# Performance work log

Hardware: AMD Instinct MI355X
Metric: run time of the kernel (lower is better)

## Reference

```python
import jax, jax.numpy as jnp
import numpy as np
from jax import lax

VOCAB = 27
N_EMBD = 512
D_MODEL = 256
PAD_IDX = 26
OUT = 1
B, T = 256, 512


def _lstm_layer(x, w_ih, w_hh, b_ih, b_hh):
    # x: [B, T, in]; w_ih: [4H, in]; w_hh: [4H, H]
    Bb = x.shape[0]
    H = w_hh.shape[1]
    # precompute input contribution to all gates for all timesteps
    xg = jnp.einsum('bti,gi->btg', x, w_ih) + b_ih + b_hh  # [B, T, 4H]

    def step(carry, xg_t):
        h, c = carry
        g = xg_t + h @ w_hh.T  # [B, 4H]
        i, f, gg, o = jnp.split(g, 4, axis=-1)  # PyTorch gate order i,f,g,o
        i = jax.nn.sigmoid(i)
        f = jax.nn.sigmoid(f)
        gg = jnp.tanh(gg)
        o = jax.nn.sigmoid(o)
        c = f * c + i * gg
        h = o * jnp.tanh(c)
        return (h, c), h

    h0 = jnp.zeros((Bb, H), dtype=x.dtype)
    c0 = jnp.zeros((Bb, H), dtype=x.dtype)
    _, ys = lax.scan(step, (h0, c0), jnp.swapaxes(xg, 0, 1))
    return jnp.swapaxes(ys, 0, 1)  # [B, T, H]


def setup_inputs() -> dict:
    key = jax.random.key(0)
    ks = jax.random.split(key, 16)
    s_e = 1.0  # nn.Embedding default init is N(0,1)
    emb = jax.random.normal(ks[0], (VOCAB, N_EMBD), dtype=jnp.float32)
    emb = emb.at[PAD_IDX].set(0.0)
    bound = 1.0 / np.sqrt(D_MODEL)

    def u(k, shape, b):
        return jax.random.uniform(k, shape, dtype=jnp.float32, minval=-b, maxval=b)

    inp = {
        'input_ids': jax.random.randint(ks[1], (B, T), 0, VOCAB, dtype=jnp.int64)
                      if jax.config.jax_enable_x64 else
                      jax.random.randint(ks[1], (B, T), 0, VOCAB).astype(jnp.int32),
        'emb': emb,
        'w_ih0': u(ks[2], (4 * D_MODEL, N_EMBD), bound),
        'w_hh0': u(ks[3], (4 * D_MODEL, D_MODEL), bound),
        'b_ih0': u(ks[4], (4 * D_MODEL,), bound),
        'b_hh0': u(ks[5], (4 * D_MODEL,), bound),
        'w_ih1': u(ks[6], (4 * D_MODEL, D_MODEL), bound),
        'w_hh1': u(ks[7], (4 * D_MODEL, D_MODEL), bound),
        'b_ih1': u(ks[8], (4 * D_MODEL,), bound),
        'b_hh1': u(ks[9], (4 * D_MODEL,), bound),
        'fc1_w': u(ks[10], (D_MODEL // 2, D_MODEL), bound),
        'fc1_b': u(ks[11], (D_MODEL // 2,), bound),
        'fc2_w': u(ks[12], (OUT, D_MODEL // 2), 1.0 / np.sqrt(D_MODEL // 2)),
        'fc2_b': u(ks[13], (OUT,), 1.0 / np.sqrt(D_MODEL // 2)),
    }
    return inp


def reference(input_ids, emb, w_ih0, w_hh0, b_ih0, b_hh0,
              w_ih1, w_hh1, b_ih1, b_hh1, fc1_w, fc1_b, fc2_w, fc2_b):
    # embedding with padding_idx: pad row forced to zero
    table = emb.at[PAD_IDX].set(0.0)
    x = table[input_ids]  # [B, T, n_embd]
    h1 = _lstm_layer(x, w_ih0, w_hh0, b_ih0, b_hh0)   # [B, T, H]
    h2 = _lstm_layer(h1, w_ih1, w_hh1, b_ih1, b_hh1)  # [B, T, H]
    last = h2[:, -1, :]                                # [B, H]
    hidden = jax.nn.relu(last @ fc1_w.T + fc1_b)
    logits = hidden @ fc2_w.T + fc2_b                  # [B, 1]
    return logits
```

## Files before the change

### kernel.cpp

```cpp
#include <hip/hip_runtime.h>

typedef unsigned short u16;
typedef unsigned int u32;
typedef unsigned long long u64;

#define BATCH 256
#define TT 512
#define HID 256
#define GATES 1024
#define NEMB 512
#define VOC 27
#define HPAD 260

__device__ __forceinline__ float bf1(u16 x){ union{u32 u; float f;} v; v.u = ((u32)x) << 16; return v.f; }
__device__ __forceinline__ u16 f2bf(float f){
  union{float f; u32 u;} v; v.f = f;
  u32 u = v.u;
  return (u16)((u + 0x7fffu + ((u >> 16) & 1u)) >> 16);
}
__device__ __forceinline__ float sigm(float x){ return 1.f / (1.f + __expf(-x)); }

__global__ void k_detect(const u16* __restrict__ b, int* __restrict__ flag) {
  int bad = 0;
  for (int k = threadIdx.x; k < 512; k += 64)
    if (((b[2 * k] >> 7) & 0xFF) >= 127) bad = 1;
  unsigned long long m = __ballot(bad);
  if (threadIdx.x == 0) flag[0] = (m != 0ULL) ? 0 : 1;
}

__global__ void k_convert(const void* __restrict__ src, float* __restrict__ dst,
                          int n, const int* __restrict__ flag) {
  int i = blockIdx.x * 256 + threadIdx.x;
  if (i >= n) return;
  dst[i] = flag[0] ? bf1(((const u16*)src)[i]) : ((const float*)src)[i];
}

__global__ void k_prep(const void* __restrict__ emb, const void* __restrict__ wih,
                       const void* __restrict__ bih, const void* __restrict__ bhh,
                       const int* __restrict__ flag, float* __restrict__ W0) {
  int idx = blockIdx.x * 256 + threadIdx.x;
  if (idx >= VOC * GATES) return;
  int v = idx >> 10, g = idx & (GATES - 1);
  int isbf = flag[0];
  float acc = isbf ? (bf1(((const u16*)bih)[g]) + bf1(((const u16*)bhh)[g]))
                   : (((const float*)bih)[g] + ((const float*)bhh)[g]);
  if (v != 26) {
    float s = 0.f;
    if (isbf) {
      const u16* e = (const u16*)emb + v * NEMB;
      const u16* w = (const u16*)wih + g * NEMB;
      for (int i = 0; i < NEMB; i++) s = fmaf(bf1(e[i]), bf1(w[i]), s);
    } else {
      const float* e = (const float*)emb + v * NEMB;
      const float* w = (const float*)wih + g * NEMB;
      for (int i = 0; i < NEMB; i++) s = fmaf(e[i], w[i], s);
    }
    acc += s;
  }
  W0[idx] = acc;
}

__global__ __launch_bounds__(1024) void k_lstm(
    const int* __restrict__ ids, const float* __restrict__ W0,
    const float* __restrict__ whh0, const float* __restrict__ wih1,
    const float* __restrict__ whh1,
    const float* __restrict__ bih1, const float* __restrict__ bhh1,
    float* __restrict__ h0a, float* __restrict__ h0b,
    float* __restrict__ h1a, float* __restrict__ h1b,
    u32* __restrict__ bar)
{
  const int tid = threadIdx.x;
  const int bid = blockIdx.x;
  const int xcd = bid & 7, m = bid >> 3;
  const int bg = xcd * 2 + (m & 1);
  const int jc = m >> 1;

  const int tb = tid & 15;
  const int rr = tid >> 4;
  const int grow = ((rr >> 4) << 8) + (jc << 4) + (rr & 15);

  __shared__ float hp0[16][HPAD];
  __shared__ float hp1[16][HPAD];
  __shared__ float gs0[64][16];
  __shared__ float gs1[64][16];
  __shared__ int   ids_s[16];

  const float* wl0 = whh0 + (size_t)grow * HID;
  const float* wi  = wih1 + (size_t)grow * HID;
  const float* wh  = whh1 + (size_t)grow * HID;
  const float bsum = bih1[grow] + bhh1[grow];

  const int lay = tid >> 8;
  const int pb = tid & 15, pj = (tid >> 4) & 15;
  const int prow = (bg * 16 + pb) * HID + (jc * 16 + pj);
  float cr = 0.f;

  u32* cnt = bar + bg * 32;

  for (int t = 0; t <= TT; ++t) {
    const float* h0p = ((t + 1) & 1) ? h0b : h0a;
    float*       h0n = (t & 1) ? h0b : h0a;
    const float* h1p = (t & 1) ? h1b : h1a;
    float*       h1n = ((t + 1) & 1) ? h1b : h1a;

    {
      const u64* s0base = (const u64*)(h0p + bg * 16 * HID);
      const u64* s1base = (const u64*)(h1p + bg * 16 * HID);
      #pragma unroll
      for (int u = 0; u < 2; ++u) {
        int e = tid + 1024 * u;
        int sb = e >> 7, sk = e & 127;
        u64 v0 = __hip_atomic_load(s0base + e, __ATOMIC_RELAXED, __HIP_MEMORY_SCOPE_AGENT);
        u64 v1 = __hip_atomic_load(s1base + e, __ATOMIC_RELAXED, __HIP_MEMORY_SCOPE_AGENT);
        *(u64*)&hp0[sb][sk * 2] = v0;
        *(u64*)&hp1[sb][sk * 2] = v1;
      }
      if (t < TT && tid < 16) ids_s[tid] = ids[(bg * 16 + tid) * TT + t];
    }
    __syncthreads();

    if (t < TT) {
      float a = W0[(size_t)ids_s[tb] * GATES + grow];
      const float* hh = hp0[tb];
      #pragma unroll 8
      for (int k = 0; k < HID; k += 4) {
        float4 q = *(const float4*)(wl0 + k);
        float4 hv = *(const float4*)(hh + k);
        a = fmaf(q.x, hv.x, a); a = fmaf(q.y, hv.y, a);
        a = fmaf(q.z, hv.z, a); a = fmaf(q.w, hv.w, a);
      }
      gs0[rr][tb] = a;
    }

    if (t > 0) {
      float e0 = bsum, e1 = 0.f;
      const float* xx = hp0[tb];
      const float* hh = hp1[tb];
      #pragma unroll 8
      for (int k = 0; k < HID; k += 4) {
        float4 qi = *(const float4*)(wi + k);
        float4 qh = *(const float4*)(wh + k);
        float4 xv = *(const float4*)(xx + k);
        float4 hv = *(const float4*)(hh + k);
        e0 = fmaf(qi.x, xv.x, e0); e0 = fmaf(qi.y, xv.y, e0);
        e0 = fmaf(qi.z, xv.z, e0); e0 = fmaf(qi.w, xv.w, e0);
        e1 = fmaf(qh.x, hv.x, e1); e1 = fmaf(qh.y, hv.y, e1);
        e1 = fmaf(qh.z, hv.z, e1); e1 = fmaf(qh.w, hv.w, e1);
      }
      gs1[rr][tb] = e0 + e1;
    }
    __syncthreads();

    if (tid < 512) {
      bool act = lay ? (t > 0) : (t < TT);
      if (act) {
        float (*gs)[16] = lay ? gs1 : gs0;
        float gi = sigm(gs[pj][pb]);
        float gf = sigm(gs[16 + pj][pb]);
        float gg = tanhf(gs[32 + pj][pb]);
        float go = sigm(gs[48 + pj][pb]);
        cr = fmaf(gf, cr, gi * gg);
        float* hn = lay ? h1n : h0n;
        __hip_atomic_store(&hn[prow], go * tanhf(cr),
                           __ATOMIC_RELAXED, __HIP_MEMORY_SCOPE_AGENT);
      }
    }

    if (t < TT) {
      __syncthreads();
      if (tid == 0) {
        __hip_atomic_fetch_add(cnt, 1u, __ATOMIC_RELAXED, __HIP_MEMORY_SCOPE_AGENT);
        u32 want = (u32)(16 * (t + 1));
        while (__hip_atomic_load(cnt, __ATOMIC_RELAXED, __HIP_MEMORY_SCOPE_AGENT) < want)
          __builtin_amdgcn_s_sleep(1);
      }
      __syncthreads();
    }
  }
}

__global__ __launch_bounds__(128) void k_fc(
    const float* __restrict__ hfin,
    const void* __restrict__ fc1w, const void* __restrict__ fc1b,
    const void* __restrict__ fc2w, const void* __restrict__ fc2b,
    const int* __restrict__ flag, void* __restrict__ out) {
  int b = blockIdx.x, j = threadIdx.x;
  __shared__ float red[128];
  const float* h = hfin + b * HID;
  int isbf = flag[0];
  float acc = isbf ? bf1(((const u16*)fc1b)[j]) : ((const float*)fc1b)[j];
  if (isbf) {
    const u16* w = (const u16*)fc1w + j * HID;
    for (int k = 0; k < HID; k++) acc = fmaf(bf1(w[k]), h[k], acc);
  } else {
    const float* w = (const float*)fc1w + j * HID;
    for (int k = 0; k < HID; k++) acc = fmaf(w[k], h[k], acc);
  }
  acc = fmaxf(acc, 0.f);
  float w2 = isbf ? bf1(((const u16*)fc2w)[j]) : ((const float*)fc2w)[j];
  red[j] = acc * w2;
  __syncthreads();
  for (int s = 64; s > 0; s >>= 1) {
    if (j < s) red[j] += red[j + s];
    __syncthreads();
  }
  if (j == 0) {
    float b2 = isbf ? bf1(((const u16*)fc2b)[0]) : ((const float*)fc2b)[0];
    float r = red[0] + b2;
    if (isbf) ((u16*)out)[b] = f2bf(r);
    else      ((float*)out)[b] = r;
  }
}

extern "C" void kernel_launch(void* const* d_in, const int* in_sizes, int n_in,
                              void* d_out, int out_size, void* d_ws, size_t ws_size,
                              hipStream_t stream) {
  const int* ids   = (const int*)d_in[0];
  const void* emb  = d_in[1];
  const void* wih0 = d_in[2];
  const void* whh0 = d_in[3];
  const void* bih0 = d_in[4];
  const void* bhh0 = d_in[5];
  const void* wih1 = d_in[6];
  const void* whh1 = d_in[7];
  const void* bih1 = d_in[8];
  const void* bhh1 = d_in[9];
  const void* fc1w = d_in[10];
  const void* fc1b = d_in[11];
  const void* fc2w = d_in[12];
  const void* fc2b = d_in[13];

  float* ws = (float*)d_ws;
  int*   flag    = (int*)ws;
  float* W0emb   = ws + 16;
  float* whh0_f  = W0emb  + VOC * GATES;
  float* wih1_f  = whh0_f + GATES * HID;
  float* whh1_f  = wih1_f + GATES * HID;
  float* bih1_f  = whh1_f + GATES * HID;
  float* bhh1_f  = bih1_f + GATES;
  float* h0A = bhh1_f + GATES;
  float* h0B = h0A + BATCH * HID;
  float* c0  = h0B + BATCH * HID;
  float* h1A = c0  + BATCH * HID;
  float* h1B = h1A + BATCH * HID;
  float* c1  = h1B + BATCH * HID;
  u32*   bar = (u32*)c0;

  k_detect<<<1, 64, 0, stream>>>((const u16*)bih0, flag);

  k_convert<<<(GATES * HID + 255) / 256, 256, 0, stream>>>(whh0, whh0_f, GATES * HID, flag);
  k_convert<<<(GATES * HID + 255) / 256, 256, 0, stream>>>(wih1, wih1_f, GATES * HID, flag);
  k_convert<<<(GATES * HID + 255) / 256, 256, 0, stream>>>(whh1, whh1_f, GATES * HID, flag);
  k_convert<<<(GATES + 255) / 256, 256, 0, stream>>>(bih1, bih1_f, GATES, flag);
  k_convert<<<(GATES + 255) / 256, 256, 0, stream>>>(bhh1, bhh1_f, GATES, flag);

  hipMemsetAsync(h0A, 0, (size_t)6 * BATCH * HID * sizeof(float), stream);

  k_prep<<<(VOC * GATES + 255) / 256, 256, 0, stream>>>(emb, wih0, bih0, bhh0, flag, W0emb);

  k_lstm<<<256, 1024, 0, stream>>>(ids, W0emb, whh0_f, wih1_f, whh1_f,
                                   bih1_f, bhh1_f, h0A, h0B, h1A, h1B, bar);

  k_fc<<<BATCH, 128, 0, stream>>>(h1B, fc1w, fc1b, fc2w, fc2b, flag, d_out);
}
```

Baseline: 13.39 ms.

## Split LSTM layer barriers and skew layer-1 to overlap with layer-0 signaling

Gives the two stacked LSTM layers separate group counters. Layer 0 signals as soon as its new hidden state is stored, so other blocks can proceed while layer 1 computes; layer 1 now runs two steps behind and reads double-buffered layer-0 states. It also preloads all token ids into shared memory, pads the gate scratch arrays to avoid bank conflicts, and uses packed 2-wide FMAs for the dot products. The price is more barriers per step, a larger shared-memory footprint (the ids table alone is about 32KB), and tricky buffer-parity correctness across the skewed layers.

```diff
diff --git a/kernel.cpp b/kernel.cpp
--- a/kernel.cpp
+++ b/kernel.cpp
@@ -3,6 +3,7 @@
 typedef unsigned short u16;
 typedef unsigned int u32;
 typedef unsigned long long u64;
+typedef float f32x2 __attribute__((ext_vector_type(2)));
 
 #define BATCH 256
 #define TT 512
@@ -19,6 +20,8 @@
   return (u16)((u + 0x7fffu + ((u >> 16) & 1u)) >> 16);
 }
 __device__ __forceinline__ float sigm(float x){ return 1.f / (1.f + __expf(-x)); }
+__device__ __forceinline__ f32x2 lo2(float4 v){ f32x2 r; r.x = v.x; r.y = v.y; return r; }
+__device__ __forceinline__ f32x2 hi2(float4 v){ f32x2 r; r.x = v.z; r.y = v.w; return r; }
 
 __global__ void k_detect(const u16* __restrict__ b, int* __restrict__ flag) {
   int bad = 0;
@@ -79,103 +82,130 @@
   const int rr = tid >> 4;
   const int grow = ((rr >> 4) << 8) + (jc << 4) + (rr & 15);
 
-  __shared__ float hp0[16][HPAD];
-  __shared__ float hp1[16][HPAD];
-  __shared__ float gs0[64][16];
-  __shared__ float gs1[64][16];
-  __shared__ int   ids_s[16];
+  __shared__ __align__(16) float hp0[2][16][HPAD];
+  __shared__ __align__(16) float hp1[16][HPAD];
+  __shared__ float gs0[64][17];
+  __shared__ float gs1[64][17];
+  __shared__ int   ids_l[16][TT + 1];
 
   const float* wl0 = whh0 + (size_t)grow * HID;
   const float* wi  = wih1 + (size_t)grow * HID;
   const float* wh  = whh1 + (size_t)grow * HID;
   const float bsum = bih1[grow] + bhh1[grow];
 
-  const int lay = tid >> 8;
-  const int pb = tid & 15, pj = (tid >> 4) & 15;
+  const int pj = tid & 15, pb = (tid >> 4) & 15;
   const int prow = (bg * 16 + pb) * HID + (jc * 16 + pj);
-  float cr = 0.f;
-
-  u32* cnt = bar + bg * 32;
-
-  for (int t = 0; t <= TT; ++t) {
-    const float* h0p = ((t + 1) & 1) ? h0b : h0a;
-    float*       h0n = (t & 1) ? h0b : h0a;
-    const float* h1p = (t & 1) ? h1b : h1a;
-    float*       h1n = ((t + 1) & 1) ? h1b : h1a;
-
-    {
-      const u64* s0base = (const u64*)(h0p + bg * 16 * HID);
-      const u64* s1base = (const u64*)(h1p + bg * 16 * HID);
+  float c0r = 0.f, c1r = 0.f;
+
+  u32* cnt0 = bar + bg * 64;
+  u32* cnt1 = cnt0 + 32;
+
+  #pragma unroll
+  for (int u = 0; u < 8; ++u) {
+    int e = tid + 1024 * u;
+    int b = e >> 9, tt = e & 511;
+    ids_l[b][tt] = ids[(bg * 16 + b) * TT + tt];
+  }
+
+  for (int t = 0; t <= TT + 1; ++t) {
+    if (tid == 0) {
+      if (t >= 1 && t <= TT) {
+        u32 want = 16u * (u32)t;
+        while (__hip_atomic_load(cnt0, __ATOMIC_RELAXED, __HIP_MEMORY_SCOPE_AGENT) < want)
+          __builtin_amdgcn_s_sleep(1);
+      }
+      if (t >= 3) {
+        u32 want = 16u * (u32)(t - 2);
+        while (__hip_atomic_load(cnt1, __ATOMIC_RELAXED, __HIP_MEMORY_SCOPE_AGENT) < want)
+          __builtin_amdgcn_s_sleep(1);
+      }
+    }
+    __syncthreads();
+
+    if (t <= TT) {
+      const float* h0p = ((t + 1) & 1) ? h0b : h0a;
+      const u64* s0 = (const u64*)(h0p + bg * 16 * HID);
+      float (*dst)[HPAD] = hp0[t & 1];
       #pragma unroll
       for (int u = 0; u < 2; ++u) {
         int e = tid + 1024 * u;
-        int sb = e >> 7, sk = e & 127;
-        u64 v0 = __hip_atomic_load(s0base + e, __ATOMIC_RELAXED, __HIP_MEMORY_SCOPE_AGENT);
-        u64 v1 = __hip_atomic_load(s1base + e, __ATOMIC_RELAXED, __HIP_MEMORY_SCOPE_AGENT);
-        *(u64*)&hp0[sb][sk * 2] = v0;
-        *(u64*)&hp1[sb][sk * 2] = v1;
-      }
-      if (t < TT && tid < 16) ids_s[tid] = ids[(bg * 16 + tid) * TT + t];
+        u64 v = __hip_atomic_load(s0 + e, __ATOMIC_RELAXED, __HIP_MEMORY_SCOPE_AGENT);
+        *(u64*)&dst[e >> 7][(e & 127) * 2] = v;
+      }
+    }
+    if (t >= 2) {
+      const float* h1p = ((t + 1) & 1) ? h1b : h1a;
+      const u64* s1 = (const u64*)(h1p + bg * 16 * HID);
+      #pragma unroll
+      for (int u = 0; u < 2; ++u) {
+        int e = tid + 1024 * u;
+        u64 v = __hip_atomic_load(s1 + e, __ATOMIC_RELAXED, __HIP_MEMORY_SCOPE_AGENT);
+        *(u64*)&hp1[e >> 7][(e & 127) * 2] = v;
+      }
     }
     __syncthreads();
 
     if (t < TT) {
-      float a = W0[(size_t)ids_s[tb] * GATES + grow];
-      const float* hh = hp0[tb];
+      float xgv = W0[(size_t)ids_l[tb][t] * GATES + grow];
+      const float4* w4 = (const float4*)wl0;
+      const float4* h4 = (const float4*)hp0[t & 1][tb];
+      f32x2 sA = {0.f, 0.f}, sB = {0.f, 0.f};
       #pragma unroll 8
-      for (int k = 0; k < HID; k += 4) {
-        float4 q = *(const float4*)(wl0 + k);
-        float4 hv = *(const float4*)(hh + k);
-        a = fmaf(q.x, hv.x, a); a = fmaf(q.y, hv.y, a);
-        a = fmaf(q.z, hv.z, a); a = fmaf(q.w, hv.w, a);
-      }
-      gs0[rr][tb] = a;
-    }
-
-    if (t > 0) {
-      float e0 = bsum, e1 = 0.f;
-      const float* xx = hp0[tb];
-      const float* hh = hp1[tb];
+      for (int k = 0; k < 64; ++k) {
+        float4 q = w4[k], hv = h4[k];
+        sA = lo2(q) * lo2(hv) + sA;
+        sB = hi2(q) * hi2(hv) + sB;
+      }
+      gs0[rr][tb] = xgv + sA.x + sA.y + sB.x + sB.y;
+    }
+    __syncthreads();
+
+    if (t < TT && tid < 256) {
+      float gi = sigm(gs0[pj][pb]);
+      float gf = sigm(gs0[16 + pj][pb]);
+      float gg = tanhf(gs0[32 + pj][pb]);
+      float go = sigm(gs0[48 + pj][pb]);
+      c0r = fmaf(gf, c0r, gi * gg);
+      float* h0n = (t & 1) ? h0b : h0a;
+      __hip_atomic_store(&h0n[prow], go * tanhf(c0r),
+                         __ATOMIC_RELAXED, __HIP_MEMORY_SCOPE_AGENT);
+    }
+    __syncthreads();
+    if (tid == 0 && t < TT)
+      __hip_atomic_fetch_add(cnt0, 1u, __ATOMIC_RELAXED, __HIP_MEMORY_SCOPE_AGENT);
+
+    if (t >= 2) {
+      const float4* wi4 = (const float4*)wi;
+      const float4* wh4 = (const float4*)wh;
+      const float4* x4  = (const float4*)hp0[(t - 1) & 1][tb];
+      const float4* h4  = (const float4*)hp1[tb];
+      f32x2 sIa = {0.f,0.f}, sIb = {0.f,0.f}, sHa = {0.f,0.f}, sHb = {0.f,0.f};
       #pragma unroll 8
-      for (int k = 0; k < HID; k += 4) {
-        float4 qi = *(const float4*)(wi + k);
-        float4 qh = *(const float4*)(wh + k);
-        float4 xv = *(const float4*)(xx + k);
-        float4 hv = *(const float4*)(hh + k);
-        e0 = fmaf(qi.x, xv.x, e0); e0 = fmaf(qi.y, xv.y, e0);
-        e0 = fmaf(qi.z, xv.z, e0); e0 = fmaf(qi.w, xv.w, e0);
-        e1 = fmaf(qh.x, hv.x, e1); e1 = fmaf(qh.y, hv.y, e1);
-        e1 = fmaf(qh.z, hv.z, e1); e1 = fmaf(qh.w, hv.w, e1);
-      }
-      gs1[rr][tb] = e0 + e1;
-    }
-    __syncthreads();
-
-    if (tid < 512) {
-      bool act = lay ? (t > 0) : (t < TT);
-      if (act) {
-        float (*gs)[16] = lay ? gs1 : gs0;
-        float gi = sigm(gs[pj][pb]);
-        float gf = sigm(gs[16 + pj][pb]);
-        float gg = tanhf(gs[32 + pj][pb]);
-        float go = sigm(gs[48 + pj][pb]);
-        cr = fmaf(gf, cr, gi * gg);
-        float* hn = lay ? h1n : h0n;
-        __hip_atomic_store(&hn[prow], go * tanhf(cr),
-                           __ATOMIC_RELAXED, __HIP_MEMORY_SCOPE_AGENT);
-      }
-    }
-
-    if (t < TT) {
-      __syncthreads();
-      if (tid == 0) {
-        __hip_atomic_fetch_add(cnt, 1u, __ATOMIC_RELAXED, __HIP_MEMORY_SCOPE_AGENT);
-        u32 want = (u32)(16 * (t + 1));
-        while (__hip_atomic_load(cnt, __ATOMIC_RELAXED, __HIP_MEMORY_SCOPE_AGENT) < want)
-          __builtin_amdgcn_s_sleep(1);
-      }
-      __syncthreads();
-    }
+      for (int k = 0; k < 64; ++k) {
+        float4 qi = wi4[k], qh = wh4[k], xv = x4[k], hv = h4[k];
+        sIa = lo2(qi) * lo2(xv) + sIa;
+        sIb = hi2(qi) * hi2(xv) + sIb;
+        sHa = lo2(qh) * lo2(hv) + sHa;
+        sHb = hi2(qh) * hi2(hv) + sHb;
+      }
+      gs1[rr][tb] = bsum + sIa.x + sIa.y + sIb.x + sIb.y
+                         + sHa.x + sHa.y + sHb.x + sHb.y;
+    }
+    __syncthreads();
+
+    if (t >= 2 && tid < 256) {
+      float gi = sigm(gs1[pj][pb]);
+      float gf = sigm(gs1[16 + pj][pb]);
+      float gg = tanhf(gs1[32 + pj][pb]);
+      float go = sigm(gs1[48 + pj][pb]);
+      c1r = fmaf(gf, c1r, gi * gg);
+      float* h1n = (t & 1) ? h1b : h1a;
+      __hip_atomic_store(&h1n[prow], go * tanhf(c1r),
+                         __ATOMIC_RELAXED, __HIP_MEMORY_SCOPE_AGENT);
+    }
+    __syncthreads();
+    if (tid == 0 && t >= 2 && t <= TT)
+      __hip_atomic_fetch_add(cnt1, 1u, __ATOMIC_RELAXED, __HIP_MEMORY_SCOPE_AGENT);
   }
 }
 
```

Measured after the change: 13.15 ms. Within noise of the previous version (-1.8%).

## Replace cross-block barrier LSTM with per-block batch ownership and local state

Applied to the files above, without the earlier changes.

The recurrent kernel now gives each of 64 blocks four full batch rows, so the hidden state stays in shared memory and the global atomic barrier between blocks is gone. Each thread computes all four gates for one hidden unit over a quarter of K, using packed float2 FMAs, and the partial sums are reduced with shuffles. Token ids are preloaded once and the two layers run back to back within each step instead of skewed by one step. In exchange, each block now streams all three full weight matrices from global memory or cache every timestep, and only 64 CUs are used.

```diff
diff --git a/kernel.cpp b/kernel.cpp
--- a/kernel.cpp
+++ b/kernel.cpp
@@ -3,6 +3,7 @@
 typedef unsigned short u16;
 typedef unsigned int u32;
 typedef unsigned long long u64;
+typedef float f32x2 __attribute__((ext_vector_type(2)));
 
 #define BATCH 256
 #define TT 512
@@ -10,7 +11,8 @@
 #define GATES 1024
 #define NEMB 512
 #define VOC 27
-#define HPAD 260
+#define KSF 68
+#define HROW 272
 
 __device__ __forceinline__ float bf1(u16 x){ union{u32 u; float f;} v; v.u = ((u32)x) << 16; return v.f; }
 __device__ __forceinline__ u16 f2bf(float f){
@@ -19,6 +21,8 @@
   return (u16)((u + 0x7fffu + ((u >> 16) & 1u)) >> 16);
 }
 __device__ __forceinline__ float sigm(float x){ return 1.f / (1.f + __expf(-x)); }
+__device__ __forceinline__ f32x2 lo2(float4 v){ f32x2 r; r.x = v.x; r.y = v.y; return r; }
+__device__ __forceinline__ f32x2 hi2(float4 v){ f32x2 r; r.x = v.z; r.y = v.w; return r; }
 
 __global__ void k_detect(const u16* __restrict__ b, int* __restrict__ flag) {
   int bad = 0;
@@ -65,116 +69,193 @@
     const float* __restrict__ whh0, const float* __restrict__ wih1,
     const float* __restrict__ whh1,
     const float* __restrict__ bih1, const float* __restrict__ bhh1,
-    float* __restrict__ h0a, float* __restrict__ h0b,
-    float* __restrict__ h1a, float* __restrict__ h1b,
-    u32* __restrict__ bar)
+    float* __restrict__ h1out)
 {
   const int tid = threadIdx.x;
   const int bid = blockIdx.x;
-  const int xcd = bid & 7, m = bid >> 3;
-  const int bg = xcd * 2 + (m & 1);
-  const int jc = m >> 1;
-
-  const int tb = tid & 15;
-  const int rr = tid >> 4;
-  const int grow = ((rr >> 4) << 8) + (jc << 4) + (rr & 15);
-
-  __shared__ float hp0[16][HPAD];
-  __shared__ float hp1[16][HPAD];
-  __shared__ float gs0[64][16];
-  __shared__ float gs1[64][16];
-  __shared__ int   ids_s[16];
-
-  const float* wl0 = whh0 + (size_t)grow * HID;
-  const float* wi  = wih1 + (size_t)grow * HID;
-  const float* wh  = whh1 + (size_t)grow * HID;
-  const float bsum = bih1[grow] + bhh1[grow];
-
-  const int lay = tid >> 8;
-  const int pb = tid & 15, pj = (tid >> 4) & 15;
-  const int prow = (bg * 16 + pb) * HID + (jc * 16 + pj);
-  float cr = 0.f;
-
-  u32* cnt = bar + bg * 32;
-
-  for (int t = 0; t <= TT; ++t) {
-    const float* h0p = ((t + 1) & 1) ? h0b : h0a;
-    float*       h0n = (t & 1) ? h0b : h0a;
-    const float* h1p = (t & 1) ? h1b : h1a;
-    float*       h1n = ((t + 1) & 1) ? h1b : h1a;
+  const int ks  = tid & 3;
+  const int j   = tid >> 2;
+  const bool owner = (ks == 0);
+
+  __shared__ __align__(16) float h0buf[2][4][HROW];
+  __shared__ __align__(16) float h1buf[2][4][HROW];
+  __shared__ int ids_l[4][TT];
+
+  {
+    float* z0 = &h0buf[0][0][0];
+    float* z1 = &h1buf[0][0][0];
+    for (int i = tid; i < 4 * HROW; i += 1024) { z0[i] = 0.f; z1[i] = 0.f; }
+  }
+  #pragma unroll
+  for (int u = 0; u < 2; ++u) {
+    int e = tid + 1024 * u;
+    int b = e >> 9, tt = e & 511;
+    ids_l[b][tt] = ids[(bid * 4 + b) * TT + tt];
+  }
+  __syncthreads();
+
+  const size_t ko = (size_t)ks * 64;
+  const float4* wl0_[4]; const float4* wi_[4]; const float4* wh_[4];
+  #pragma unroll
+  for (int g = 0; g < 4; ++g) {
+    size_t r = (size_t)(g * 256 + j) * HID + ko;
+    wl0_[g] = (const float4*)(whh0 + r);
+    wi_[g]  = (const float4*)(wih1 + r);
+    wh_[g]  = (const float4*)(whh1 + r);
+  }
+  float bs[4];
+  #pragma unroll
+  for (int g = 0; g < 4; ++g) bs[g] = bih1[g * 256 + j] + bhh1[g * 256 + j];
+
+  const int jm = ((j >> 6) * KSF) + (j & 63);
+  float c0r[4] = {0.f, 0.f, 0.f, 0.f};
+  float c1r[4] = {0.f, 0.f, 0.f, 0.f};
+
+  for (int t = 0; t < TT; ++t) {
+    const int pc = t & 1, pn = pc ^ 1;
+
+    float xg[4][4];
+    if (owner) {
+      #pragma unroll
+      for (int b = 0; b < 4; ++b) {
+        const float* xr = W0 + (size_t)ids_l[b][t] * GATES + j;
+        xg[0][b] = xr[0];   xg[1][b] = xr[256];
+        xg[2][b] = xr[512]; xg[3][b] = xr[768];
+      }
+    }
 
     {
-      const u64* s0base = (const u64*)(h0p + bg * 16 * HID);
-      const u64* s1base = (const u64*)(h1p + bg * 16 * HID);
-      #pragma unroll
-      for (int u = 0; u < 2; ++u) {
-        int e = tid + 1024 * u;
-        int sb = e >> 7, sk = e & 127;
-        u64 v0 = __hip_atomic_load(s0base + e, __ATOMIC_RELAXED, __HIP_MEMORY_SCOPE_AGENT);
-        u64 v1 = __hip_atomic_load(s1base + e, __ATOMIC_RELAXED, __HIP_MEMORY_SCOPE_AGENT);
-        *(u64*)&hp0[sb][sk * 2] = v0;
-        *(u64*)&hp1[sb][sk * 2] = v1;
-      }
-      if (t < TT && tid < 16) ids_s[tid] = ids[(bg * 16 + tid) * TT + t];
+      const float4* hb[4];
+      #pragma unroll
+      for (int b = 0; b < 4; ++b) hb[b] = (const float4*)&h0buf[pc][b][ks * KSF];
+      f32x2 a[4][4];
+      #pragma unroll
+      for (int g = 0; g < 4; ++g)
+        #pragma unroll
+        for (int b = 0; b < 4; ++b) { a[g][b].x = 0.f; a[g][b].y = 0.f; }
+      #pragma unroll 4
+      for (int k = 0; k < 16; ++k) {
+        float4 w0 = wl0_[0][k], w1 = wl0_[1][k], w2 = wl0_[2][k], w3 = wl0_[3][k];
+        float4 x0 = hb[0][k], x1 = hb[1][k], x2 = hb[2][k], x3 = hb[3][k];
+        a[0][0] = lo2(w0)*lo2(x0) + a[0][0]; a[0][0] = hi2(w0)*hi2(x0) + a[0][0];
+        a[0][1] = lo2(w0)*lo2(x1) + a[0][1]; a[0][1] = hi2(w0)*hi2(x1) + a[0][1];
+        a[0][2] = lo2(w0)*lo2(x2) + a[0][2]; a[0][2] = hi2(w0)*hi2(x2) + a[0][2];
+        a[0][3] = lo2(w0)*lo2(x3) + a[0][3]; a[0][3] = hi2(w0)*hi2(x3) + a[0][3];
+        a[1][0] = lo2(w1)*lo2(x0) + a[1][0]; a[1][0] = hi2(w1)*hi2(x0) + a[1][0];
+        a[1][1] = lo2(w1)*lo2(x1) + a[1][1]; a[1][1] = hi2(w1)*hi2(x1) + a[1][1];
+        a[1][2] = lo2(w1)*lo2(x2) + a[1][2]; a[1][2] = hi2(w1)*hi2(x2) + a[1][2];
+        a[1][3] = lo2(w1)*lo2(x3) + a[1][3]; a[1][3] = hi2(w1)*hi2(x3) + a[1][3];
+        a[2][0] = lo2(w2)*lo2(x0) + a[2][0]; a[2][0] = hi2(w2)*hi2(x0) + a[2][0];
+        a[2][1] = lo2(w2)*lo2(x1) + a[2][1]; a[2][1] = hi2(w2)*hi2(x1) + a[2][1];
+        a[2][2] = lo2(w2)*lo2(x2) + a[2][2]; a[2][2] = hi2(w2)*hi2(x2) + a[2][2];
+        a[2][3] = lo2(w2)*lo2(x3) + a[2][3]; a[2][3] = hi2(w2)*hi2(x3) + a[2][3];
+        a[3][0] = lo2(w3)*lo2(x0) + a[3][0]; a[3][0] = hi2(w3)*hi2(x0) + a[3][0];
+        a[3][1] = lo2(w3)*lo2(x1) + a[3][1]; a[3][1] = hi2(w3)*hi2(x1) + a[3][1];
+        a[3][2] = lo2(w3)*lo2(x2) + a[3][2]; a[3][2] = hi2(w3)*hi2(x2) + a[3][2];
+        a[3][3] = lo2(w3)*lo2(x3) + a[3][3]; a[3][3] = hi2(w3)*hi2(x3) + a[3][3];
+      }
+      float s[4][4];
+      #pragma unroll
+      for (int g = 0; g < 4; ++g)
+        #pragma unroll
+        for (int b = 0; b < 4; ++b) {
+          float v = a[g][b].x + a[g][b].y;
+          v += __shfl_xor(v, 1);
+          v += __shfl_xor(v, 2);
+          s[g][b] = v;
+        }
+      if (owner) {
+        #pragma unroll
+        for (int b = 0; b < 4; ++b) {
+          float gi = sigm(s[0][b] + xg[0][b]);
+          float gf = sigm(s[1][b] + xg[1][b]);
+          float gg = tanhf(s[2][b] + xg[2][b]);
+          float go = sigm(s[3][b] + xg[3][b]);
+          c0r[b] = fmaf(gf, c0r[b], gi * gg);
+          h0buf[pn][b][jm] = go * tanhf(c0r[b]);
+        }
+      }
     }
     __syncthreads();
 
-    if (t < TT) {
-      float a = W0[(size_t)ids_s[tb] * GATES + grow];
-      const float* hh = hp0[tb];
-      #pragma unroll 8
-      for (int k = 0; k < HID; k += 4) {
-        float4 q = *(const float4*)(wl0 + k);
-        float4 hv = *(const float4*)(hh + k);
-        a = fmaf(q.x, hv.x, a); a = fmaf(q.y, hv.y, a);
-        a = fmaf(q.z, hv.z, a); a = fmaf(q.w, hv.w, a);
-      }
-      gs0[rr][tb] = a;
-    }
-
-    if (t > 0) {
-      float e0 = bsum, e1 = 0.f;
-      const float* xx = hp0[tb];
-      const float* hh = hp1[tb];
-      #pragma unroll 8
-      for (int k = 0; k < HID; k += 4) {
-        float4 qi = *(const float4*)(wi + k);
-        float4 qh = *(const float4*)(wh + k);
-        float4 xv = *(const float4*)(xx + k);
-        float4 hv = *(const float4*)(hh + k);
-        e0 = fmaf(qi.x, xv.x, e0); e0 = fmaf(qi.y, xv.y, e0);
-        e0 = fmaf(qi.z, xv.z, e0); e0 = fmaf(qi.w, xv.w, e0);
-        e1 = fmaf(qh.x, hv.x, e1); e1 = fmaf(qh.y, hv.y, e1);
-        e1 = fmaf(qh.z, hv.z, e1); e1 = fmaf(qh.w, hv.w, e1);
-      }
-      gs1[rr][tb] = e0 + e1;
-    }
-    __syncthreads();
-
-    if (tid < 512) {
-      bool act = lay ? (t > 0) : (t < TT);
-      if (act) {
-        float (*gs)[16] = lay ? gs1 : gs0;
-        float gi = sigm(gs[pj][pb]);
-        float gf = sigm(gs[16 + pj][pb]);
-        float gg = tanhf(gs[32 + pj][pb]);
-        float go = sigm(gs[48 + pj][pb]);
-        cr = fmaf(gf, cr, gi * gg);
-        float* hn = lay ? h1n : h0n;
-        __hip_atomic_store(&hn[prow], go * tanhf(cr),
-                           __ATOMIC_RELAXED, __HIP_MEMORY_SCOPE_AGENT);
-      }
-    }
-
-    if (t < TT) {
-      __syncthreads();
-      if (tid == 0) {
-        __hip_atomic_fetch_add(cnt, 1u, __ATOMIC_RELAXED, __HIP_MEMORY_SCOPE_AGENT);
-        u32 want = (u32)(16 * (t + 1));
-        while (__hip_atomic_load(cnt, __ATOMIC_RELAXED, __HIP_MEMORY_SCOPE_AGENT) < want)
-          __builtin_amdgcn_s_sleep(1);
-      }
-      __syncthreads();
+    {
+      const float4* xb[4]; const float4* hb[4];
+      #pragma unroll
+      for (int b = 0; b < 4; ++b) {
+        xb[b] = (const float4*)&h0buf[pn][b][ks * KSF];
+        hb[b] = (const float4*)&h1buf[pc][b][ks * KSF];
+      }
+      f32x2 a[4][4];
+      #pragma unroll
+      for (int g = 0; g < 4; ++g)
+        #pragma unroll
+        for (int b = 0; b < 4; ++b) { a[g][b].x = 0.f; a[g][b].y = 0.f; }
+      #pragma unroll 2
+      for (int k = 0; k < 16; ++k) {
+        float4 x0 = xb[0][k], x1 = xb[1][k], x2 = xb[2][k], x3 = xb[3][k];
+        {
+          float4 w0 = wi_[0][k], w1 = wi_[1][k], w2 = wi_[2][k], w3 = wi_[3][k];
+          a[0][0] = lo2(w0)*lo2(x0) + a[0][0]; a[0][0] = hi2(w0)*hi2(x0) + a[0][0];
+          a[0][1] = lo2(w0)*lo2(x1) + a[0][1]; a[0][1] = hi2(w0)*hi2(x1) + a[0][1];
+          a[0][2] = lo2(w0)*lo2(x2) + a[0][2]; a[0][2] = hi2(w0)*hi2(x2) + a[0][2];
+          a[0][3] = lo2(w0)*lo2(x3) + a[0][3]; a[0][3] = hi2(w0)*hi2(x3) + a[0][3];
+          a[1][0] = lo2(w1)*lo2(x0) + a[1][0]; a[1][0] = hi2(w1)*hi2(x0) + a[1][0];
+          a[1][1] = lo2(w1)*lo2(x1) + a[1][1]; a[1][1] = hi2(w1)*hi2(x1) + a[1][1];
+          a[1][2] = lo2(w1)*lo2(x2) + a[1][2]; a[1][2] = hi2(w1)*hi2(x2) + a[1][2];
+          a[1][3] = lo2(w1)*lo2(x3) + a[1][3]; a[1][3] = hi2(w1)*hi2(x3) + a[1][3];
+          a[2][0] = lo2(w2)*lo2(x0) + a[2][0]; a[2][0] = hi2(w2)*hi2(x0) + a[2][0];
+          a[2][1] = lo2(w2)*lo2(x1) + a[2][1]; a[2][1] = hi2(w2)*hi2(x1) + a[2][1];
+          a[2][2] = lo2(w2)*lo2(x2) + a[2][2]; a[2][2] = hi2(w2)*hi2(x2) + a[2][2];
+          a[2][3] = lo2(w2)*lo2(x3) + a[2][3]; a[2][3] = hi2(w2)*hi2(x3) + a[2][3];
+          a[3][0] = lo2(w3)*lo2(x0) + a[3][0]; a[3][0] = hi2(w3)*hi2(x0) + a[3][0];
+          a[3][1] = lo2(w3)*lo2(x1) + a[3][1]; a[3][1] = hi2(w3)*hi2(x1) + a[3][1];
+          a[3][2] = lo2(w3)*lo2(x2) + a[3][2]; a[3][2] = hi2(w3)*hi2(x2) + a[3][2];
+          a[3][3] = lo2(w3)*lo2(x3) + a[3][3]; a[3][3] = hi2(w3)*hi2(x3) + a[3][3];
+        }
+        float4 h0v = hb[0][k], h1v = hb[1][k], h2v = hb[2][k], h3v = hb[3][k];
+        {
+          float4 w0 = wh_[0][k], w1 = wh_[1][k], w2 = wh_[2][k], w3 = wh_[3][k];
+          a[0][0] = lo2(w0)*lo2(h0v) + a[0][0]; a[0][0] = hi2(w0)*hi2(h0v) + a[0][0];
+          a[0][1] = lo2(w0)*lo2(h1v) + a[0][1]; a[0][1] = hi2(w0)*hi2(h1v) + a[0][1];
+          a[0][2] = lo2(w0)*lo2(h2v) + a[0][2]; a[0][2] = hi2(w0)*hi2(h2v) + a[0][2];
+          a[0][3] = lo2(w0)*lo2(h3v) + a[0][3]; a[0][3] = hi2(w0)*hi2(h3v) + a[0][3];
+          a[1][0] = lo2(w1)*lo2(h0v) + a[1][0]; a[1][0] = hi2(w1)*hi2(h0v) + a[1][0];
+          a[1][1] = lo2(w1)*lo2(h1v) + a[1][1]; a[1][1] = hi2(w1)*hi2(h1v) + a[1][1];
+          a[1][2] = lo2(w1)*lo2(h2v) + a[1][2]; a[1][2] = hi2(w1)*hi2(h2v) + a[1][2];
+          a[1][3] = lo2(w1)*lo2(h3v) + a[1][3]; a[1][3] = hi2(w1)*hi2(h3v) + a[1][3];
+          a[2][0] = lo2(w2)*lo2(h0v) + a[2][0]; a[2][0] = hi2(w2)*hi2(h0v) + a[2][0];
+          a[2][1] = lo2(w2)*lo2(h1v) + a[2][1]; a[2][1] = hi2(w2)*hi2(h1v) + a[2][1];
+          a[2][2] = lo2(w2)*lo2(h2v) + a[2][2]; a[2][2] = hi2(w2)*hi2(h2v) + a[2][2];
+          a[2][3] = lo2(w2)*lo2(h3v) + a[2][3]; a[2][3] = hi2(w2)*hi2(h3v) + a[2][3];
+          a[3][0] = lo2(w3)*lo2(h0v) + a[3][0]; a[3][0] = hi2(w3)*hi2(h0v) + a[3][0];
+          a[3][1] = lo2(w3)*lo2(h1v) + a[3][1]; a[3][1] = hi2(w3)*hi2(h1v) + a[3][1];
+          a[3][2] = lo2(w3)*lo2(h2v) + a[3][2]; a[3][2] = hi2(w3)*hi2(h2v) + a[3][2];
+          a[3][3] = lo2(w3)*lo2(h3v) + a[3][3]; a[3][3] = hi2(w3)*hi2(h3v) + a[3][3];
+        }
+      }
+      float s[4][4];
+      #pragma unroll
+      for (int g = 0; g < 4; ++g)
+        #pragma unroll
+        for (int b = 0; b < 4; ++b) {
+          float v = a[g][b].x + a[g][b].y;
+          v += __shfl_xor(v, 1);
+          v += __shfl_xor(v, 2);
+          s[g][b] = v;
+        }
+      if (owner) {
+        #pragma unroll
+        for (int b = 0; b < 4; ++b) {
+          float gi = sigm(s[0][b] + bs[0]);
+          float gf = sigm(s[1][b] + bs[1]);
+          float gg = tanhf(s[2][b] + bs[2]);
+          float go = sigm(s[3][b] + bs[3]);
+          c1r[b] = fmaf(gf, c1r[b], gi * gg);
+          float hv = go * tanhf(c1r[b]);
+          h1buf[pn][b][jm] = hv;
+          if (t == TT - 1) h1out[(bid * 4 + b) * HID + j] = hv;
+        }
+      }
     }
   }
 }
@@ -238,13 +319,7 @@
   float* whh1_f  = wih1_f + GATES * HID;
   float* bih1_f  = whh1_f + GATES * HID;
   float* bhh1_f  = bih1_f + GATES;
-  float* h0A = bhh1_f + GATES;
-  float* h0B = h0A + BATCH * HID;
-  float* c0  = h0B + BATCH * HID;
-  float* h1A = c0  + BATCH * HID;
-  float* h1B = h1A + BATCH * HID;
-  float* c1  = h1B + BATCH * HID;
-  u32*   bar = (u32*)c0;
+  float* h1B     = bhh1_f + GATES;
 
   k_detect<<<1, 64, 0, stream>>>((const u16*)bih0, flag);
 
@@ -254,12 +329,10 @@
   k_convert<<<(GATES + 255) / 256, 256, 0, stream>>>(bih1, bih1_f, GATES, flag);
   k_convert<<<(GATES + 255) / 256, 256, 0, stream>>>(bhh1, bhh1_f, GATES, flag);
 
-  hipMemsetAsync(h0A, 0, (size_t)6 * BATCH * HID * sizeof(float), stream);
-
   k_prep<<<(VOC * GATES + 255) / 256, 256, 0, stream>>>(emb, wih0, bih0, bhh0, flag, W0emb);
 
-  k_lstm<<<256, 1024, 0, stream>>>(ids, W0emb, whh0_f, wih1_f, whh1_f,
-                                   bih1_f, bhh1_f, h0A, h0B, h1A, h1B, bar);
+  k_lstm<<<64, 1024, 0, stream>>>(ids, W0emb, whh0_f, wih1_f, whh1_f,
+                                  bih1_f, bhh1_f, h1B);
 
   k_fc<<<BATCH, 128, 0, stream>>>(h1B, fc1w, fc1b, fc2w, fc2b, flag, d_out);
 }
```

Result: slower. 50.94 ms (+280.4%).
